# Performance work log

Hardware: AMD Instinct MI355X
Metric: run time of the kernel (lower is better)

## Reference

```python
import jax, jax.numpy as jnp
import numpy as np

BATCH, SEQ, IN, HID, CLS = 512, 1024, 64, 256, 10

def setup_inputs() -> dict:
    key = jax.random.key(0)
    k1, k2, k3, k4, k5 = jax.random.split(key, 5)
    s_ih = 1.0 / np.sqrt(IN + HID)
    s_ho = 1.0 / np.sqrt(HID)
    return {
        "inputs": jax.random.normal(k1, (BATCH, SEQ, IN), dtype=jnp.float32),
        "W_ih": jax.random.normal(k2, (IN + HID, HID), dtype=jnp.float32) * s_ih,
        "b_ih": jax.random.normal(k3, (HID,), dtype=jnp.float32) * s_ih,
        "W_ho": jax.random.normal(k4, (HID, CLS), dtype=jnp.float32) * s_ho,
        "b_ho": jax.random.normal(k5, (CLS,), dtype=jnp.float32) * s_ho,
    }

def reference(inputs, W_ih, b_ih, W_ho, b_ho):
    # Elman RNN: hidden_{t} = tanh([x_t, hidden_{t-1}] @ W_ih + b_ih)
    B, S, I = inputs.shape
    H = W_ih.shape[1]
    # split W_ih into input and hidden blocks (equivalent to concat+matmul)
    Wx = W_ih[:I]      # (I, H)
    Wh = W_ih[I:]      # (H, H)
    h0 = jnp.zeros((B, H), dtype=inputs.dtype)
    # precompute input projections for all timesteps at once: (B, S, H)
    xproj = jnp.einsum('bsi,ih->bsh', inputs, Wx) + b_ih

    def step(h, xp_t):
        h_new = jnp.tanh(xp_t + h @ Wh)
        return h_new, None

    h_final, _ = jax.lax.scan(step, h0, jnp.swapaxes(xproj, 0, 1))  # scan over time
    return h_final @ W_ho + b_ho  # (B, CLS)
```

## Files before the change

### kernel.cpp

```cpp
#include <hip/hip_runtime.h>
#include <hip/hip_bf16.h>


#define BATCH 512
#define SEQ   1024
#define INP   64
#define HID   256
#define CLS   10
#define NTHREADS 512
#define TSCALE 2.8853900817779268f

typedef short bf16x8 __attribute__((ext_vector_type(8)));
typedef float f32x4  __attribute__((ext_vector_type(4)));

static __device__ __forceinline__ unsigned short f2bf(float f) {
  __hip_bfloat16 h = __float2bfloat16(f);
  return *reinterpret_cast<unsigned short*>(&h);
}
static __device__ __forceinline__ float bf2f(unsigned short b) {
  union { unsigned int u; float f; } v; v.u = ((unsigned int)b) << 16;
  return v.f;
}
static __device__ __forceinline__ unsigned int cvt_pk_bf16(float lo, float hi) {
  unsigned int r;
  asm("v_cvt_pk_bf16_f32 %0, %1, %2" : "=v"(r) : "v"(lo), "v"(hi));
  return r;
}
static __device__ __forceinline__ float fast_exp2(float x) {
#if __has_builtin(__builtin_amdgcn_exp2f)
  return __builtin_amdgcn_exp2f(x);
#else
  return __exp2f(x);
#endif
}
static __device__ __forceinline__ float fast_rcp(float x) {
#if __has_builtin(__builtin_amdgcn_rcpf)
  return __builtin_amdgcn_rcpf(x);
#else
  return 1.0f / x;
#endif
}
static __device__ __forceinline__ float tanh_scaled(float s) {
  return 1.0f - 2.0f * fast_rcp(1.0f + fast_exp2(s));
}

#define MFMA16(A, B, C) __builtin_amdgcn_mfma_f32_16x16x32_bf16(A, B, C, 0, 0, 0)

#define BARRIER() asm volatile("s_waitcnt lgkmcnt(0)\n\ts_barrier" ::: "memory")

#define STEP(T, CUR, XR) do {                                                   \
        \
    if (wave == 0) {                                                            \
      ((unsigned int*)sX[(CUR) ^ 1])[(xcp >> 4) * 32 + xrow * 16 + (xcp & 15)]  \
          = cvt_pk_bf16(XR.x, XR.y);                                            \
      int tn_ = (T) + 3; tn_ = tn_ < SEQ ? tn_ : SEQ - 1;                       \
      XR = *(const float2*)&xstage[(size_t)tn_ * INP];                          \
    }                                                                           \
    f32x4 acc0a = {bias0, bias0, bias0, bias0};                                 \
    f32x4 acc1a = {bias1, bias1, bias1, bias1};                                 \
    f32x4 acc0b = {0.f, 0.f, 0.f, 0.f};                                         \
    f32x4 acc1b = {0.f, 0.f, 0.f, 0.f};                                         \
                         \
    if (frow < 2) {                                                             \
      aP0 = *(const bf16x8*)&sX[CUR][0][frow][g8];                              \
      aP1 = *(const bf16x8*)&sX[CUR][1][frow][g8];                              \
      aQ0 = *(const bf16x8*)&sH[CUR][0][frow][g8];                              \
      aQ1 = *(const bf16x8*)&sH[CUR][1][frow][g8];                              \
    }                                                                           \
    __builtin_amdgcn_s_setprio(1);                                              \
    acc0a = MFMA16(aP0, bw[0][0], acc0a); acc1a = MFMA16(aP0, bw[0][1], acc1a); \
    acc0b = MFMA16(aP1, bw[1][0], acc0b); acc1b = MFMA16(aP1, bw[1][1], acc1b); \
    __builtin_amdgcn_sched_barrier(0);                                          \
    if (frow < 2) {                                                             \
      aP0 = *(const bf16x8*)&sH[CUR][2][frow][g8];                              \
      aP1 = *(const bf16x8*)&sH[CUR][3][frow][g8];                              \
    }                                                                           \
    acc0a = MFMA16(aQ0, bw[2][0], acc0a); acc1a = MFMA16(aQ0, bw[2][1], acc1a); \
    acc0b = MFMA16(aQ1, bw[3][0], acc0b); acc1b = MFMA16(aQ1, bw[3][1], acc1b); \
    __builtin_amdgcn_sched_barrier(0);                                          \
    if (frow < 2) {                                                             \
      aQ0 = *(const bf16x8*)&sH[CUR][4][frow][g8];                              \
      aQ1 = *(const bf16x8*)&sH[CUR][5][frow][g8];                              \
    }                                                                           \
    acc0a = MFMA16(aP0, bw[4][0], acc0a); acc1a = MFMA16(aP0, bw[4][1], acc1a); \
    acc0b = MFMA16(aP1, bw[5][0], acc0b); acc1b = MFMA16(aP1, bw[5][1], acc1b); \
    __builtin_amdgcn_sched_barrier(0);                                          \
    if (frow < 2) {                                                             \
      aP0 = *(const bf16x8*)&sH[CUR][6][frow][g8];                              \
      aP1 = *(const bf16x8*)&sH[CUR][7][frow][g8];                              \
    }                                                                           \
    acc0a = MFMA16(aQ0, bw[6][0], acc0a); acc1a = MFMA16(aQ0, bw[6][1], acc1a); \
    acc0b = MFMA16(aQ1, bw[7][0], acc0b); acc1b = MFMA16(aQ1, bw[7][1], acc1b); \
    __builtin_amdgcn_sched_barrier(0);                                          \
    acc0a = MFMA16(aP0, bw[8][0], acc0a); acc1a = MFMA16(aP0, bw[8][1], acc1a); \
    acc0b = MFMA16(aP1, bw[9][0], acc0b); acc1b = MFMA16(aP1, bw[9][1], acc1b); \
    __builtin_amdgcn_s_setprio(0);                                              \
            \
    float t00 = tanh_scaled(acc0a[0] + acc0b[0]);       \
    float t10 = tanh_scaled(acc1a[0] + acc1b[0]);       \
    float t01 = tanh_scaled(acc0a[1] + acc0b[1]);       \
    float t11 = tanh_scaled(acc1a[1] + acc1b[1]);       \
    if (g == 0) {                                                               \
      unsigned int* hd_ = (unsigned int*)sH[(CUR) ^ 1];                         \
      hd_[wave * 32 + frow]      = cvt_pk_bf16(t00, t10);            \
      hd_[wave * 32 + 16 + frow] = cvt_pk_bf16(t01, t11);            \
    }                                                                           \
    BARRIER();                                                                  \
  } while (0)

__global__ __launch_bounds__(NTHREADS, 2)
void rnn_scan_kernel(const float* __restrict__ x,
                     const float* __restrict__ W_ih,
                     const float* __restrict__ b_ih,
                     const float* __restrict__ W_ho,
                     const float* __restrict__ b_ho,
                     float* __restrict__ out) {
  __shared__ __align__(16) unsigned short sH[2][8][2][32];
  __shared__ __align__(16) unsigned short sX[2][2][2][32];

  const int tid  = threadIdx.x;
  const int lane = tid & 63;
  const int wave = tid >> 6;
  const int b0   = blockIdx.x * 2;

  const int g    = (lane >> 4) & 3;
  const int g8   = g * 8;
  const int frow = lane & 15;

  bf16x8 bw[10][2];
  const int colE = 32 * wave + 2 * frow;
  const float bias0 = b_ih[colE] * TSCALE;
  const float bias1 = b_ih[colE + 1] * TSCALE;
#pragma unroll
  for (int q = 0; q < 2; ++q) {
#pragma unroll
    for (int kt = 0; kt < 10; ++kt) {
      bf16x8 v;
#pragma unroll
      for (int i = 0; i < 8; ++i)
        v[i] = (short)f2bf(W_ih[(size_t)(kt * 32 + g * 8 + i) * HID + colE + q] * TSCALE);
      bw[kt][q] = v;
    }
  }

  const int xrow = lane >> 5, xcp = lane & 31;
  const float* xstage = x + (size_t)(b0 + xrow) * SEQ * INP + xcp * 2;
  float2 xrA = make_float2(0.f, 0.f), xrB = make_float2(0.f, 0.f);

  bf16x8 aP0 = {}, aP1 = {}, aQ0 = {}, aQ1 = {};

  if (tid < 256) ((unsigned int*)sH[0])[tid] = 0u;
  if (wave == 0) {
    float2 v0 = *(const float2*)&xstage[0];
    ((unsigned int*)sX[0])[(xcp >> 4) * 32 + xrow * 16 + (xcp & 15)]
        = cvt_pk_bf16(v0.x, v0.y);
    xrA = *(const float2*)&xstage[(size_t)1 * INP];
    xrB = *(const float2*)&xstage[(size_t)2 * INP];
  }
  BARRIER();

#pragma unroll 1
  for (int t = 0; t < SEQ; t += 2) {
    STEP(t,     0, xrA);
    STEP(t + 1, 1, xrB);
  }

  if (tid < 2 * CLS) {
    const int r = tid / CLS, cl = tid - r * CLS;
    float s = b_ho[cl];
#pragma unroll 8
    for (int k = 0; k < HID; ++k)
      s += bf2f(sH[0][k >> 5][r][k & 31]) * W_ho[(size_t)k * CLS + cl];
    out[(size_t)(b0 + r) * CLS + cl] = s;
  }
}

extern "C" void kernel_launch(void* const* d_in, const int* in_sizes, int n_in,
                              void* d_out, int out_size, void* d_ws, size_t ws_size,
                              hipStream_t stream) {
  const float* x    = (const float*)d_in[0];
  const float* W_ih = (const float*)d_in[1];
  const float* b_ih = (const float*)d_in[2];
  const float* W_ho = (const float*)d_in[3];
  const float* b_ho = (const float*)d_in[4];
  float* out = (float*)d_out;

  rnn_scan_kernel<<<BATCH / 2, NTHREADS, 0, stream>>>(x, W_ih, b_ih, W_ho, b_ho, out);
}
```

Before: 529.3 us.

## Process one batch row per block and launch a block per row

Each block now handles a single batch row instead of two, and the grid doubles to one block per row. Shared-memory hidden and input buffers shrink, and only one MFMA row slot is filled. The goal is to let two independent recurrence chains share each CU so their barrier and latency stalls overlap. In exchange, each CU issues twice the MFMA and LDS work, and half the MFMA rows are wasted on padding.

```diff
diff --git a/kernel.cpp b/kernel.cpp
--- a/kernel.cpp
+++ b/kernel.cpp
@@ -50,8 +50,8 @@
 
 #define STEP(T, CUR, XR) do {                                                   \
         \
-    if (wave == 0) {                                                            \
-      ((unsigned int*)sX[(CUR) ^ 1])[(xcp >> 4) * 32 + xrow * 16 + (xcp & 15)]  \
+    if (wave == 0 && lane < 32) {                                               \
+      ((unsigned int*)sX[(CUR) ^ 1])[(lane >> 4) * 16 + (lane & 15)]            \
           = cvt_pk_bf16(XR.x, XR.y);                                            \
       int tn_ = (T) + 3; tn_ = tn_ < SEQ ? tn_ : SEQ - 1;                       \
       XR = *(const float2*)&xstage[(size_t)tn_ * INP];                          \
@@ -60,34 +60,34 @@
     f32x4 acc1a = {bias1, bias1, bias1, bias1};                                 \
     f32x4 acc0b = {0.f, 0.f, 0.f, 0.f};                                         \
     f32x4 acc1b = {0.f, 0.f, 0.f, 0.f};                                         \
-                         \
-    if (frow < 2) {                                                             \
-      aP0 = *(const bf16x8*)&sX[CUR][0][frow][g8];                              \
-      aP1 = *(const bf16x8*)&sX[CUR][1][frow][g8];                              \
-      aQ0 = *(const bf16x8*)&sH[CUR][0][frow][g8];                              \
-      aQ1 = *(const bf16x8*)&sH[CUR][1][frow][g8];                              \
+                     \
+    if (frow == 0) {                                                            \
+      aP0 = *(const bf16x8*)&sX[CUR][0][g8];                                    \
+      aP1 = *(const bf16x8*)&sX[CUR][1][g8];                                    \
+      aQ0 = *(const bf16x8*)&sH[CUR][0][g8];                                    \
+      aQ1 = *(const bf16x8*)&sH[CUR][1][g8];                                    \
     }                                                                           \
     __builtin_amdgcn_s_setprio(1);                                              \
     acc0a = MFMA16(aP0, bw[0][0], acc0a); acc1a = MFMA16(aP0, bw[0][1], acc1a); \
     acc0b = MFMA16(aP1, bw[1][0], acc0b); acc1b = MFMA16(aP1, bw[1][1], acc1b); \
     __builtin_amdgcn_sched_barrier(0);                                          \
-    if (frow < 2) {                                                             \
-      aP0 = *(const bf16x8*)&sH[CUR][2][frow][g8];                              \
-      aP1 = *(const bf16x8*)&sH[CUR][3][frow][g8];                              \
+    if (frow == 0) {                                                            \
+      aP0 = *(const bf16x8*)&sH[CUR][2][g8];                                    \
+      aP1 = *(const bf16x8*)&sH[CUR][3][g8];                                    \
     }                                                                           \
     acc0a = MFMA16(aQ0, bw[2][0], acc0a); acc1a = MFMA16(aQ0, bw[2][1], acc1a); \
     acc0b = MFMA16(aQ1, bw[3][0], acc0b); acc1b = MFMA16(aQ1, bw[3][1], acc1b); \
     __builtin_amdgcn_sched_barrier(0);                                          \
-    if (frow < 2) {                                                             \
-      aQ0 = *(const bf16x8*)&sH[CUR][4][frow][g8];                              \
-      aQ1 = *(const bf16x8*)&sH[CUR][5][frow][g8];                              \
+    if (frow == 0) {                                                            \
+      aQ0 = *(const bf16x8*)&sH[CUR][4][g8];                                    \
+      aQ1 = *(const bf16x8*)&sH[CUR][5][g8];                                    \
     }                                                                           \
     acc0a = MFMA16(aP0, bw[4][0], acc0a); acc1a = MFMA16(aP0, bw[4][1], acc1a); \
     acc0b = MFMA16(aP1, bw[5][0], acc0b); acc1b = MFMA16(aP1, bw[5][1], acc1b); \
     __builtin_amdgcn_sched_barrier(0);                                          \
-    if (frow < 2) {                                                             \
-      aP0 = *(const bf16x8*)&sH[CUR][6][frow][g8];                              \
-      aP1 = *(const bf16x8*)&sH[CUR][7][frow][g8];                              \
+    if (frow == 0) {                                                            \
+      aP0 = *(const bf16x8*)&sH[CUR][6][g8];                                    \
+      aP1 = *(const bf16x8*)&sH[CUR][7][g8];                                    \
     }                                                                           \
     acc0a = MFMA16(aQ0, bw[6][0], acc0a); acc1a = MFMA16(aQ0, bw[6][1], acc1a); \
     acc0b = MFMA16(aQ1, bw[7][0], acc0b); acc1b = MFMA16(aQ1, bw[7][1], acc1b); \
@@ -95,15 +95,12 @@
     acc0a = MFMA16(aP0, bw[8][0], acc0a); acc1a = MFMA16(aP0, bw[8][1], acc1a); \
     acc0b = MFMA16(aP1, bw[9][0], acc0b); acc1b = MFMA16(aP1, bw[9][1], acc1b); \
     __builtin_amdgcn_s_setprio(0);                                              \
-            \
-    float t00 = tanh_scaled(acc0a[0] + acc0b[0]);       \
-    float t10 = tanh_scaled(acc1a[0] + acc1b[0]);       \
-    float t01 = tanh_scaled(acc0a[1] + acc0b[1]);       \
-    float t11 = tanh_scaled(acc1a[1] + acc1b[1]);       \
+                     \
+    float t00 = tanh_scaled(acc0a[0] + acc0b[0]);             \
+    float t10 = tanh_scaled(acc1a[0] + acc1b[0]);             \
     if (g == 0) {                                                               \
-      unsigned int* hd_ = (unsigned int*)sH[(CUR) ^ 1];                         \
-      hd_[wave * 32 + frow]      = cvt_pk_bf16(t00, t10);            \
-      hd_[wave * 32 + 16 + frow] = cvt_pk_bf16(t01, t11);            \
+                   \
+      ((unsigned int*)sH[(CUR) ^ 1])[wave * 16 + frow] = cvt_pk_bf16(t00, t10); \
     }                                                                           \
     BARRIER();                                                                  \
   } while (0)
@@ -115,13 +112,13 @@
                      const float* __restrict__ W_ho,
                      const float* __restrict__ b_ho,
                      float* __restrict__ out) {
-  __shared__ __align__(16) unsigned short sH[2][8][2][32];
-  __shared__ __align__(16) unsigned short sX[2][2][2][32];
+  __shared__ __align__(16) unsigned short sH[2][8][32];
+  __shared__ __align__(16) unsigned short sX[2][2][32];
 
   const int tid  = threadIdx.x;
   const int lane = tid & 63;
   const int wave = tid >> 6;
-  const int b0   = blockIdx.x * 2;
+  const int row  = blockIdx.x;
 
   const int g    = (lane >> 4) & 3;
   const int g8   = g * 8;
@@ -143,16 +140,15 @@
     }
   }
 
-  const int xrow = lane >> 5, xcp = lane & 31;
-  const float* xstage = x + (size_t)(b0 + xrow) * SEQ * INP + xcp * 2;
+  const float* xstage = x + (size_t)row * SEQ * INP + lane * 2;
   float2 xrA = make_float2(0.f, 0.f), xrB = make_float2(0.f, 0.f);
 
   bf16x8 aP0 = {}, aP1 = {}, aQ0 = {}, aQ1 = {};
 
-  if (tid < 256) ((unsigned int*)sH[0])[tid] = 0u;
-  if (wave == 0) {
+  if (tid < 128) ((unsigned int*)sH[0])[tid] = 0u;
+  if (wave == 0 && lane < 32) {
     float2 v0 = *(const float2*)&xstage[0];
-    ((unsigned int*)sX[0])[(xcp >> 4) * 32 + xrow * 16 + (xcp & 15)]
+    ((unsigned int*)sX[0])[(lane >> 4) * 16 + (lane & 15)]
         = cvt_pk_bf16(v0.x, v0.y);
     xrA = *(const float2*)&xstage[(size_t)1 * INP];
     xrB = *(const float2*)&xstage[(size_t)2 * INP];
@@ -165,13 +161,13 @@
     STEP(t + 1, 1, xrB);
   }
 
-  if (tid < 2 * CLS) {
-    const int r = tid / CLS, cl = tid - r * CLS;
+  if (tid < CLS) {
+    const int cl = tid;
     float s = b_ho[cl];
 #pragma unroll 8
     for (int k = 0; k < HID; ++k)
-      s += bf2f(sH[0][k >> 5][r][k & 31]) * W_ho[(size_t)k * CLS + cl];
-    out[(size_t)(b0 + r) * CLS + cl] = s;
+      s += bf2f(sH[0][k >> 5][k & 31]) * W_ho[(size_t)k * CLS + cl];
+    out[(size_t)row * CLS + cl] = s;
   }
 }
 
@@ -185,5 +181,5 @@
   const float* b_ho = (const float*)d_in[4];
   float* out = (float*)d_out;
 
-  rnn_scan_kernel<<<BATCH / 2, NTHREADS, 0, stream>>>(x, W_ih, b_ih, W_ho, b_ho, out);
+  rnn_scan_kernel<<<BATCH, NTHREADS, 0, stream>>>(x, W_ih, b_ih, W_ho, b_ho, out);
 }
```

After: 991.6 us. +87.4%, slower.

## Halve waves per block, giving each wave 64 hidden columns

Applied to the files above, without the earlier changes.

The recurrent step now runs on 4 waves instead of 8. Each wave computes 64 hidden columns using four accumulator chains, with twice as many weight fragments held in registers. Launch bounds change to a single wave per EU so the larger register footprint fits. The split-K accumulator pairs and the setprio hints are removed. The goal is cheaper per-step barriers and fewer waves to synchronise, at the cost of longer per-wave MFMA dependency chains and twice the tanh work per wave on the serial critical path.

```diff
diff --git a/kernel.cpp b/kernel.cpp
--- a/kernel.cpp
+++ b/kernel.cpp
@@ -7,7 +7,7 @@
 #define INP   64
 #define HID   256
 #define CLS   10
-#define NTHREADS 512
+#define NTHREADS 256
 #define TSCALE 2.8853900817779268f
 
 typedef short bf16x8 __attribute__((ext_vector_type(8)));
@@ -48,18 +48,24 @@
 
 #define BARRIER() asm volatile("s_waitcnt lgkmcnt(0)\n\ts_barrier" ::: "memory")
 
+#define MF8(AF, KT)                                                             \
+    acc00 = MFMA16(AF, bw[KT][0][0], acc00);                                    \
+    acc01 = MFMA16(AF, bw[KT][0][1], acc01);                                    \
+    acc10 = MFMA16(AF, bw[KT][1][0], acc10);                                    \
+    acc11 = MFMA16(AF, bw[KT][1][1], acc11)
+
 #define STEP(T, CUR, XR) do {                                                   \
         \
     if (wave == 0) {                                                            \
-      ((unsigned int*)sX[(CUR) ^ 1])[(xcp >> 4) * 32 + xrow * 16 + (xcp & 15)]  \
+      ((unsigned int*)sX[(CUR) ^ 1])[((xcp >> 4) * 2 + xrow) * 16 + (xcp & 15)] \
           = cvt_pk_bf16(XR.x, XR.y);                                            \
       int tn_ = (T) + 3; tn_ = tn_ < SEQ ? tn_ : SEQ - 1;                       \
       XR = *(const float2*)&xstage[(size_t)tn_ * INP];                          \
     }                                                                           \
-    f32x4 acc0a = {bias0, bias0, bias0, bias0};                                 \
-    f32x4 acc1a = {bias1, bias1, bias1, bias1};                                 \
-    f32x4 acc0b = {0.f, 0.f, 0.f, 0.f};                                         \
-    f32x4 acc1b = {0.f, 0.f, 0.f, 0.f};                                         \
+    f32x4 acc00 = {bias00, bias00, 0.f, 0.f};                                   \
+    f32x4 acc01 = {bias01, bias01, 0.f, 0.f};                                   \
+    f32x4 acc10 = {bias10, bias10, 0.f, 0.f};                                   \
+    f32x4 acc11 = {bias11, bias11, 0.f, 0.f};                                   \
                          \
     if (frow < 2) {                                                             \
       aP0 = *(const bf16x8*)&sX[CUR][0][frow][g8];                              \
@@ -67,48 +73,48 @@
       aQ0 = *(const bf16x8*)&sH[CUR][0][frow][g8];                              \
       aQ1 = *(const bf16x8*)&sH[CUR][1][frow][g8];                              \
     }                                                                           \
-    __builtin_amdgcn_s_setprio(1);                                              \
-    acc0a = MFMA16(aP0, bw[0][0], acc0a); acc1a = MFMA16(aP0, bw[0][1], acc1a); \
-    acc0b = MFMA16(aP1, bw[1][0], acc0b); acc1b = MFMA16(aP1, bw[1][1], acc1b); \
+    MF8(aP0, 0); MF8(aP1, 1);                                                   \
     __builtin_amdgcn_sched_barrier(0);                                          \
     if (frow < 2) {                                                             \
       aP0 = *(const bf16x8*)&sH[CUR][2][frow][g8];                              \
       aP1 = *(const bf16x8*)&sH[CUR][3][frow][g8];                              \
     }                                                                           \
-    acc0a = MFMA16(aQ0, bw[2][0], acc0a); acc1a = MFMA16(aQ0, bw[2][1], acc1a); \
-    acc0b = MFMA16(aQ1, bw[3][0], acc0b); acc1b = MFMA16(aQ1, bw[3][1], acc1b); \
+    MF8(aQ0, 2); MF8(aQ1, 3);                                                   \
     __builtin_amdgcn_sched_barrier(0);                                          \
     if (frow < 2) {                                                             \
       aQ0 = *(const bf16x8*)&sH[CUR][4][frow][g8];                              \
       aQ1 = *(const bf16x8*)&sH[CUR][5][frow][g8];                              \
     }                                                                           \
-    acc0a = MFMA16(aP0, bw[4][0], acc0a); acc1a = MFMA16(aP0, bw[4][1], acc1a); \
-    acc0b = MFMA16(aP1, bw[5][0], acc0b); acc1b = MFMA16(aP1, bw[5][1], acc1b); \
+    MF8(aP0, 4); MF8(aP1, 5);                                                   \
     __builtin_amdgcn_sched_barrier(0);                                          \
     if (frow < 2) {                                                             \
       aP0 = *(const bf16x8*)&sH[CUR][6][frow][g8];                              \
       aP1 = *(const bf16x8*)&sH[CUR][7][frow][g8];                              \
     }                                                                           \
-    acc0a = MFMA16(aQ0, bw[6][0], acc0a); acc1a = MFMA16(aQ0, bw[6][1], acc1a); \
-    acc0b = MFMA16(aQ1, bw[7][0], acc0b); acc1b = MFMA16(aQ1, bw[7][1], acc1b); \
-    __builtin_amdgcn_sched_barrier(0);                                          \
-    acc0a = MFMA16(aP0, bw[8][0], acc0a); acc1a = MFMA16(aP0, bw[8][1], acc1a); \
-    acc0b = MFMA16(aP1, bw[9][0], acc0b); acc1b = MFMA16(aP1, bw[9][1], acc1b); \
-    __builtin_amdgcn_s_setprio(0);                                              \
+    MF8(aQ0, 6); MF8(aQ1, 7);                                                   \
+    __builtin_amdgcn_sched_barrier(0);                                          \
+    MF8(aP0, 8); MF8(aP1, 9);                                                   \
             \
-    float t00 = tanh_scaled(acc0a[0] + acc0b[0]);       \
-    float t10 = tanh_scaled(acc1a[0] + acc1b[0]);       \
-    float t01 = tanh_scaled(acc0a[1] + acc0b[1]);       \
-    float t11 = tanh_scaled(acc1a[1] + acc1b[1]);       \
+    float t000 = tanh_scaled(acc00[0]);               \
+    float t010 = tanh_scaled(acc01[0]);               \
+    float t100 = tanh_scaled(acc10[0]);               \
+    float t110 = tanh_scaled(acc11[0]);               \
+    float t001 = tanh_scaled(acc00[1]);                      \
+    float t011 = tanh_scaled(acc01[1]);                                         \
+    float t101 = tanh_scaled(acc10[1]);                                         \
+    float t111 = tanh_scaled(acc11[1]);                                         \
     if (g == 0) {                                                               \
       unsigned int* hd_ = (unsigned int*)sH[(CUR) ^ 1];                         \
-      hd_[wave * 32 + frow]      = cvt_pk_bf16(t00, t10);            \
-      hd_[wave * 32 + 16 + frow] = cvt_pk_bf16(t01, t11);            \
+      hd_[((2 * wave + 0) * 2 + 0) * 16 + frow] = cvt_pk_bf16(t000, t010);      \
+      hd_[((2 * wave + 0) * 2 + 1) * 16 + frow] = cvt_pk_bf16(t001, t011);      \
+      hd_[((2 * wave + 1) * 2 + 0) * 16 + frow] = cvt_pk_bf16(t100, t110);      \
+      hd_[((2 * wave + 1) * 2 + 1) * 16 + frow] = cvt_pk_bf16(t101, t111);      \
     }                                                                           \
     BARRIER();                                                                  \
   } while (0)
 
-__global__ __launch_bounds__(NTHREADS, 2)
+__global__ __launch_bounds__(NTHREADS)
+__attribute__((amdgpu_waves_per_eu(1)))
 void rnn_scan_kernel(const float* __restrict__ x,
                      const float* __restrict__ W_ih,
                      const float* __restrict__ b_ih,
@@ -127,19 +133,26 @@
   const int g8   = g * 8;
   const int frow = lane & 15;
 
-  bf16x8 bw[10][2];
-  const int colE = 32 * wave + 2 * frow;
-  const float bias0 = b_ih[colE] * TSCALE;
-  const float bias1 = b_ih[colE + 1] * TSCALE;
-#pragma unroll
-  for (int q = 0; q < 2; ++q) {
-#pragma unroll
-    for (int kt = 0; kt < 10; ++kt) {
-      bf16x8 v;
-#pragma unroll
-      for (int i = 0; i < 8; ++i)
-        v[i] = (short)f2bf(W_ih[(size_t)(kt * 32 + g * 8 + i) * HID + colE + q] * TSCALE);
-      bw[kt][q] = v;
+  bf16x8 bw[10][2][2];
+  float bias00, bias01, bias10, bias11;
+#pragma unroll
+  for (int p = 0; p < 2; ++p) {
+#pragma unroll
+    for (int q = 0; q < 2; ++q) {
+      const int col = 64 * wave + 32 * p + 2 * frow + q;
+      const float bb = b_ih[col] * TSCALE;
+      if (p == 0 && q == 0) bias00 = bb;
+      if (p == 0 && q == 1) bias01 = bb;
+      if (p == 1 && q == 0) bias10 = bb;
+      if (p == 1 && q == 1) bias11 = bb;
+#pragma unroll
+      for (int kt = 0; kt < 10; ++kt) {
+        bf16x8 v;
+#pragma unroll
+        for (int i = 0; i < 8; ++i)
+          v[i] = (short)f2bf(W_ih[(size_t)(kt * 32 + g * 8 + i) * HID + col] * TSCALE);
+        bw[kt][p][q] = v;
+      }
     }
   }
 
@@ -152,7 +165,7 @@
   if (tid < 256) ((unsigned int*)sH[0])[tid] = 0u;
   if (wave == 0) {
     float2 v0 = *(const float2*)&xstage[0];
-    ((unsigned int*)sX[0])[(xcp >> 4) * 32 + xrow * 16 + (xcp & 15)]
+    ((unsigned int*)sX[0])[((xcp >> 4) * 2 + xrow) * 16 + (xcp & 15)]
         = cvt_pk_bf16(v0.x, v0.y);
     xrA = *(const float2*)&xstage[(size_t)1 * INP];
     xrB = *(const float2*)&xstage[(size_t)2 * INP];
```

Result: slower. 598.5 us (+13.1%).

## Double waves per block so each wave computes sixteen hidden columns

Applied to the files above, without the earlier changes.

Raises the block to 1024 threads (16 waves) and gives each wave 16 hidden columns instead of 32. Per-wave weight registers and MFMA issues per step are halved, and each lane writes one bf16 hidden value instead of a packed pair. The aim is to shorten each serial recurrence step by spreading the MFMA work over more waves on the CU. In exchange, every per-step barrier now synchronises twice as many waves, and the s_setprio hints are removed.

```diff
diff --git a/kernel.cpp b/kernel.cpp
--- a/kernel.cpp
+++ b/kernel.cpp
@@ -7,7 +7,7 @@
 #define INP   64
 #define HID   256
 #define CLS   10
-#define NTHREADS 512
+#define NTHREADS 1024
 #define TSCALE 2.8853900817779268f
 
 typedef short bf16x8 __attribute__((ext_vector_type(8)));
@@ -51,15 +51,13 @@
 #define STEP(T, CUR, XR) do {                                                   \
         \
     if (wave == 0) {                                                            \
-      ((unsigned int*)sX[(CUR) ^ 1])[(xcp >> 4) * 32 + xrow * 16 + (xcp & 15)]  \
+      ((unsigned int*)sX[(CUR) ^ 1])[((xcp >> 4) * 2 + xrow) * 16 + (xcp & 15)] \
           = cvt_pk_bf16(XR.x, XR.y);                                            \
       int tn_ = (T) + 3; tn_ = tn_ < SEQ ? tn_ : SEQ - 1;                       \
       XR = *(const float2*)&xstage[(size_t)tn_ * INP];                          \
     }                                                                           \
-    f32x4 acc0a = {bias0, bias0, bias0, bias0};                                 \
-    f32x4 acc1a = {bias1, bias1, bias1, bias1};                                 \
-    f32x4 acc0b = {0.f, 0.f, 0.f, 0.f};                                         \
-    f32x4 acc1b = {0.f, 0.f, 0.f, 0.f};                                         \
+    f32x4 acca = {bias, bias, bias, bias};                                      \
+    f32x4 accb = {0.f, 0.f, 0.f, 0.f};                                          \
                          \
     if (frow < 2) {                                                             \
       aP0 = *(const bf16x8*)&sX[CUR][0][frow][g8];                              \
@@ -67,48 +65,45 @@
       aQ0 = *(const bf16x8*)&sH[CUR][0][frow][g8];                              \
       aQ1 = *(const bf16x8*)&sH[CUR][1][frow][g8];                              \
     }                                                                           \
-    __builtin_amdgcn_s_setprio(1);                                              \
-    acc0a = MFMA16(aP0, bw[0][0], acc0a); acc1a = MFMA16(aP0, bw[0][1], acc1a); \
-    acc0b = MFMA16(aP1, bw[1][0], acc0b); acc1b = MFMA16(aP1, bw[1][1], acc1b); \
+    acca = MFMA16(aP0, bw[0], acca);                                            \
+    accb = MFMA16(aP1, bw[1], accb);                                            \
     __builtin_amdgcn_sched_barrier(0);                                          \
     if (frow < 2) {                                                             \
       aP0 = *(const bf16x8*)&sH[CUR][2][frow][g8];                              \
       aP1 = *(const bf16x8*)&sH[CUR][3][frow][g8];                              \
     }                                                                           \
-    acc0a = MFMA16(aQ0, bw[2][0], acc0a); acc1a = MFMA16(aQ0, bw[2][1], acc1a); \
-    acc0b = MFMA16(aQ1, bw[3][0], acc0b); acc1b = MFMA16(aQ1, bw[3][1], acc1b); \
+    acca = MFMA16(aQ0, bw[2], acca);                                            \
+    accb = MFMA16(aQ1, bw[3], accb);                                            \
     __builtin_amdgcn_sched_barrier(0);                                          \
     if (frow < 2) {                                                             \
       aQ0 = *(const bf16x8*)&sH[CUR][4][frow][g8];                              \
       aQ1 = *(const bf16x8*)&sH[CUR][5][frow][g8];                              \
     }                                                                           \
-    acc0a = MFMA16(aP0, bw[4][0], acc0a); acc1a = MFMA16(aP0, bw[4][1], acc1a); \
-    acc0b = MFMA16(aP1, bw[5][0], acc0b); acc1b = MFMA16(aP1, bw[5][1], acc1b); \
+    acca = MFMA16(aP0, bw[4], acca);                                            \
+    accb = MFMA16(aP1, bw[5], accb);                                            \
     __builtin_amdgcn_sched_barrier(0);                                          \
     if (frow < 2) {                                                             \
       aP0 = *(const bf16x8*)&sH[CUR][6][frow][g8];                              \
       aP1 = *(const bf16x8*)&sH[CUR][7][frow][g8];                              \
     }                                                                           \
-    acc0a = MFMA16(aQ0, bw[6][0], acc0a); acc1a = MFMA16(aQ0, bw[6][1], acc1a); \
-    acc0b = MFMA16(aQ1, bw[7][0], acc0b); acc1b = MFMA16(aQ1, bw[7][1], acc1b); \
+    acca = MFMA16(aQ0, bw[6], acca);                                            \
+    accb = MFMA16(aQ1, bw[7], accb);                                            \
     __builtin_amdgcn_sched_barrier(0);                                          \
-    acc0a = MFMA16(aP0, bw[8][0], acc0a); acc1a = MFMA16(aP0, bw[8][1], acc1a); \
-    acc0b = MFMA16(aP1, bw[9][0], acc0b); acc1b = MFMA16(aP1, bw[9][1], acc1b); \
-    __builtin_amdgcn_s_setprio(0);                                              \
+    acca = MFMA16(aP0, bw[8], acca);                                            \
+    accb = MFMA16(aP1, bw[9], accb);                                            \
             \
-    float t00 = tanh_scaled(acc0a[0] + acc0b[0]);       \
-    float t10 = tanh_scaled(acc1a[0] + acc1b[0]);       \
-    float t01 = tanh_scaled(acc0a[1] + acc0b[1]);       \
-    float t11 = tanh_scaled(acc1a[1] + acc1b[1]);       \
+    float t0 = tanh_scaled(acca[0] + accb[0]);             \
+    float t1 = tanh_scaled(acca[1] + accb[1]);             \
     if (g == 0) {                                                               \
-      unsigned int* hd_ = (unsigned int*)sH[(CUR) ^ 1];                         \
-      hd_[wave * 32 + frow]      = cvt_pk_bf16(t00, t10);            \
-      hd_[wave * 32 + 16 + frow] = cvt_pk_bf16(t01, t11);            \
+      unsigned short* hd_ = (unsigned short*)sH[(CUR) ^ 1];                     \
+            \
+      hd_[(wave >> 1) * 64 + 0 * 32 + (wave & 1) * 16 + frow] = f2bf(t0);       \
+      hd_[(wave >> 1) * 64 + 1 * 32 + (wave & 1) * 16 + frow] = f2bf(t1);       \
     }                                                                           \
     BARRIER();                                                                  \
   } while (0)
 
-__global__ __launch_bounds__(NTHREADS, 2)
+__global__ __launch_bounds__(NTHREADS, 1)
 void rnn_scan_kernel(const float* __restrict__ x,
                      const float* __restrict__ W_ih,
                      const float* __restrict__ b_ih,
@@ -127,20 +122,16 @@
   const int g8   = g * 8;
   const int frow = lane & 15;
 
-  bf16x8 bw[10][2];
-  const int colE = 32 * wave + 2 * frow;
-  const float bias0 = b_ih[colE] * TSCALE;
-  const float bias1 = b_ih[colE + 1] * TSCALE;
+  bf16x8 bw[10];
+  const int col = 16 * wave + frow;
+  const float bias = b_ih[col] * TSCALE;
 #pragma unroll
-  for (int q = 0; q < 2; ++q) {
+  for (int kt = 0; kt < 10; ++kt) {
+    bf16x8 v;
 #pragma unroll
-    for (int kt = 0; kt < 10; ++kt) {
-      bf16x8 v;
-#pragma unroll
-      for (int i = 0; i < 8; ++i)
-        v[i] = (short)f2bf(W_ih[(size_t)(kt * 32 + g * 8 + i) * HID + colE + q] * TSCALE);
-      bw[kt][q] = v;
-    }
+    for (int i = 0; i < 8; ++i)
+      v[i] = (short)f2bf(W_ih[(size_t)(kt * 32 + g * 8 + i) * HID + col] * TSCALE);
+    bw[kt] = v;
   }
 
   const int xrow = lane >> 5, xcp = lane & 31;
@@ -152,7 +143,7 @@
   if (tid < 256) ((unsigned int*)sH[0])[tid] = 0u;
   if (wave == 0) {
     float2 v0 = *(const float2*)&xstage[0];
-    ((unsigned int*)sX[0])[(xcp >> 4) * 32 + xrow * 16 + (xcp & 15)]
+    ((unsigned int*)sX[0])[((xcp >> 4) * 2 + xrow) * 16 + (xcp & 15)]
         = cvt_pk_bf16(v0.x, v0.y);
     xrA = *(const float2*)&xstage[(size_t)1 * INP];
     xrB = *(const float2*)&xstage[(size_t)2 * INP];
```

Result: slower. 547.7 us (+3.5%).
